# Optimization experiments

Hardware: AMD Instinct MI355X
Metric: run time of the kernel (lower is better)

The kernel has to match this reference:

```python
import jax, jax.numpy as jnp
import numpy as np

POS_IN, HID, DIR_IN, SIG_OUT, COL_OUT = 63, 128, 27, 1, 3
TOTAL = POS_IN * HID + HID + HID * SIG_OUT + SIG_OUT + (HID + DIR_IN) * COL_OUT + COL_OUT  # 8717
B, N = 32, 65536


def positional_encoding(x, num_freqs):
    # x: [..., D] -> [..., D + D*2*num_freqs]
    freqs = 2.0 ** jnp.arange(num_freqs, dtype=x.dtype)  # [F]
    x_exp = x[..., None] * freqs                          # [..., D, F]
    flat = x_exp.reshape(*x.shape[:-1], -1)               # [..., D*F]
    return jnp.concatenate([x, jnp.sin(flat), jnp.cos(flat)], axis=-1)


def setup_inputs() -> dict:
    key = jax.random.key(0)
    k1, k2, k3 = jax.random.split(key, 3)
    params = jax.random.normal(k1, (B, TOTAL), dtype=jnp.float32) * 0.1
    points = jax.random.uniform(k2, (B, N, 3), dtype=jnp.float32, minval=-1.0, maxval=1.0)
    dirs = jax.random.uniform(k3, (B, N, 3), dtype=jnp.float32, minval=-1.0, maxval=1.0)
    return {"params": params, "points": points, "dirs": dirs}


def _unpack(params):
    b = params.shape[0]
    i = 0
    pw = params[:, i:i + POS_IN * HID].reshape(b, HID, POS_IN); i += POS_IN * HID
    pb = params[:, i:i + HID]; i += HID
    sw = params[:, i:i + HID * SIG_OUT].reshape(b, SIG_OUT, HID); i += HID * SIG_OUT
    sb = params[:, i:i + SIG_OUT]; i += SIG_OUT
    cin = HID + DIR_IN
    cw = params[:, i:i + cin * COL_OUT].reshape(b, COL_OUT, cin); i += cin * COL_OUT
    cb = params[:, i:i + COL_OUT]
    return pw, pb, sw, sb, cw, cb


def reference(params, points, dirs):
    pw, pb, sw, sb, cw, cb = _unpack(params)
    pos_enc = positional_encoding(points, 10)   # [B,N,63]
    dir_enc = positional_encoding(dirs, 4)      # [B,N,27]
    h = jnp.einsum('bni,bhi->bnh', pos_enc, pw) + pb[:, None, :]  # [B,N,128]
    h = jax.nn.relu(h)
    sigma = jnp.einsum('bnh,boh->bno', h, sw) + sb[:, None, :]    # [B,N,1]
    h_dir = jnp.concatenate([h, dir_enc], axis=-1)                # [B,N,155]
    color = jnp.einsum('bnc,boc->bno', h_dir, cw) + cb[:, None, :]  # [B,N,3]
    color = jax.nn.sigmoid(color)
    return jnp.concatenate([color, sigma], axis=-1)               # [B,N,4]
```

## Files before the change

### kernel.cpp

```cpp
#include <hip/hip_runtime.h>

#define POS_IN 63
#define HID 128
#define TOTAL 8789
#define NB 32
#define NPTS 65536

#define PB_OFF 8064
#define SW_OFF 8192
#define SB_OFF 8320
#define CW_OFF 8321
#define CB_OFF 8786

#define BLOCKS_PER_BATCH 32
#define PTS_PER_BLOCK (NPTS / BLOCKS_PER_BATCH)
#define ITERS (PTS_PER_BLOCK / 256)

typedef __attribute__((ext_vector_type(8))) short s16x8;
typedef __attribute__((ext_vector_type(4))) float f32x4;
typedef __bf16 bf16x2 __attribute__((ext_vector_type(2)));

__device__ __forceinline__ unsigned short f2bf(float v) {
    unsigned u = __builtin_bit_cast(unsigned, v);
    unsigned r = 0x7fffu + ((u >> 16) & 1u);
    return (unsigned short)((u + r) >> 16);
}
__device__ __forceinline__ unsigned pk2(float a, float b) {
    bf16x2 v;
    v[0] = (__bf16)a;
    v[1] = (__bf16)b;
    return __builtin_bit_cast(unsigned, v);
}

__global__ __launch_bounds__(256, 2) void nerf_mlp_kernel(
        const float* __restrict__ params,
        const float* __restrict__ points,
        const float* __restrict__ dirs,
        float* __restrict__ out)
{
    __shared__ __align__(16) unsigned char smem[37888];
    unsigned short* stage = (unsigned short*)smem;

    const int tid = threadIdx.x;
    const int lane = tid & 63;
    const int wid = tid >> 6;
    const int b = blockIdx.y;
    const float* P = params + (size_t)b * TOTAL;

    for (int idx = tid; idx < 8064; idx += 256) {
        int n = idx / 63;
        int k = idx - n * 63;
        stage[n * 72 + k] = f2bf(P[idx]);
        if (k == 0) stage[n * 72 + 63] = f2bf(P[PB_OFF + n]);
    }
    __syncthreads();

    const int c = lane & 15;
    const int kg = lane >> 4;

    s16x8 wB[8][2];
    #pragma unroll
    for (int nt = 0; nt < 8; ++nt) {
        #pragma unroll
        for (int kh = 0; kh < 2; ++kh) {
            int n = nt * 16 + c;
            int k = kh * 32 + kg * 8;
            uint4 raw = *(const uint4*)&stage[n * 72 + k];
            wB[nt][kh] = __builtin_bit_cast(s16x8, raw);
        }
    }
    __syncthreads();

    s16x8 wB2[4];
    #pragma unroll
    for (int m = 0; m < 4; ++m) {
        unsigned d0 = 0, d1 = 0, d2 = 0, d3 = 0;
        if (c < 4) {
            const int base = (c == 3) ? SW_OFF : (CW_OFF + c * 155);
            const int h0 = m * 32 + kg * 8;
            d0 = pk2(P[base + h0 + 0], P[base + h0 + 1]);
            d1 = pk2(P[base + h0 + 2], P[base + h0 + 3]);
            d2 = pk2(P[base + h0 + 4], P[base + h0 + 5]);
            d3 = pk2(P[base + h0 + 6], P[base + h0 + 7]);
        }
        uint4 dd = make_uint4(d0, d1, d2, d3);
        wB2[m] = __builtin_bit_cast(s16x8, dd);
    }

    const int ch = lane & 3;
    const float cbias = P[ch < 3 ? (CB_OFF + ch) : SB_OFF];

    unsigned char* encb = smem + wid * 8192;
    unsigned char* hbuf = smem + 32768 + wid * 1280;

    const size_t bpts = (size_t)b * NPTS;
    const int n0b = blockIdx.x * PTS_PER_BLOCK;

    for (int it = 0; it < ITERS; ++it) {
        const int n0 = n0b + it * 256 + wid * 64;
        const int p = n0 + lane;

        const float* pp = points + (bpts + p) * 3;
        float x = pp[0], y = pp[1], z = pp[2];
        const float* dd = dirs + (bpts + p) * 3;
        float dx = dd[0], dy = dd[1], dz = dd[2];

        float e[64];
        e[0] = x; e[1] = y; e[2] = z; e[63] = 1.0f;
        #pragma unroll
        for (int i = 0; i < 3; ++i) {
            float v = (i == 0) ? x : (i == 1) ? y : z;
            float s = __sinf(v), co = __cosf(v);
            e[3 + i * 10] = s; e[33 + i * 10] = co;
            #pragma unroll
            for (int f = 1; f < 10; ++f) {
                float ns = 2.f * s * co;
                float nc = 1.f - 2.f * s * s;
                s = ns; co = nc;
                e[3 + i * 10 + f] = s;
                e[33 + i * 10 + f] = co;
            }
        }

        float cp0 = 0.f, cp1 = 0.f, cp2 = 0.f;
        #pragma unroll
        for (int i = 0; i < 3; ++i) {
            float v = (i == 0) ? dx : (i == 1) ? dy : dz;
            cp0 = fmaf(v, P[CW_OFF + 128 + i], cp0);
            cp1 = fmaf(v, P[CW_OFF + 155 + 128 + i], cp1);
            cp2 = fmaf(v, P[CW_OFF + 310 + 128 + i], cp2);
            float s = __sinf(v), co = __cosf(v);
            #pragma unroll
            for (int f = 0; f < 4; ++f) {
                if (f > 0) {
                    float ns = 2.f * s * co;
                    float nc = 1.f - 2.f * s * s;
                    s = ns; co = nc;
                }
                int si = 128 + 3 + i * 4 + f;
                int ci = 128 + 15 + i * 4 + f;
                cp0 = fmaf(s, P[CW_OFF + si], cp0);
                cp1 = fmaf(s, P[CW_OFF + 155 + si], cp1);
                cp2 = fmaf(s, P[CW_OFF + 310 + si], cp2);
                cp0 = fmaf(co, P[CW_OFF + ci], cp0);
                cp1 = fmaf(co, P[CW_OFF + 155 + ci], cp1);
                cp2 = fmaf(co, P[CW_OFF + 310 + ci], cp2);
            }
        }

        #pragma unroll
        for (int kq = 0; kq < 8; ++kq) {
            uint4 q;
            q.x = pk2(e[kq * 8 + 0], e[kq * 8 + 1]);
            q.y = pk2(e[kq * 8 + 2], e[kq * 8 + 3]);
            q.z = pk2(e[kq * 8 + 4], e[kq * 8 + 5]);
            q.w = pk2(e[kq * 8 + 6], e[kq * 8 + 7]);
            *(uint4*)(encb + kq * 1024 + lane * 16) = q;
        }

        float* outp = out + (bpts + n0) * 4;

        #pragma unroll
        for (int t = 0; t < 4; ++t) {
            uint4 a0r = *(const uint4*)(encb + kg * 1024 + (t * 16 + c) * 16);
            uint4 a1r = *(const uint4*)(encb + (4 + kg) * 1024 + (t * 16 + c) * 16);
            s16x8 A0 = __builtin_bit_cast(s16x8, a0r);
            s16x8 A1 = __builtin_bit_cast(s16x8, a1r);

            f32x4 acc[8];
            #pragma unroll
            for (int nt = 0; nt < 8; ++nt) {
                acc[nt] = (f32x4){0.f, 0.f, 0.f, 0.f};
                acc[nt] = __builtin_amdgcn_mfma_f32_16x16x32_bf16(wB[nt][0], A0, acc[nt], 0, 0, 0);
                acc[nt] = __builtin_amdgcn_mfma_f32_16x16x32_bf16(wB[nt][1], A1, acc[nt], 0, 0, 0);
            }
            #pragma unroll
            for (int nt = 0; nt < 8; ++nt)
                #pragma unroll
                for (int j = 0; j < 4; ++j)
                    acc[nt][j] = fmaxf(acc[nt][j], 0.f);

            f32x4 acc2 = (f32x4){0.f, 0.f, 0.f, 0.f};
            #pragma unroll
            for (int m = 0; m < 4; ++m) {
                unsigned q0 = pk2(acc[2 * m][0], acc[2 * m][1]);
                unsigned q1 = pk2(acc[2 * m][2], acc[2 * m][3]);
                unsigned q2 = pk2(acc[2 * m + 1][0], acc[2 * m + 1][1]);
                unsigned q3 = pk2(acc[2 * m + 1][2], acc[2 * m + 1][3]);
                *(uint2*)(hbuf + c * 80 + kg * 8)      = make_uint2(q0, q1);
                *(uint2*)(hbuf + c * 80 + 32 + kg * 8) = make_uint2(q2, q3);
                uint4 ar = *(const uint4*)(hbuf + c * 80 + kg * 16);
                s16x8 A2 = __builtin_bit_cast(s16x8, ar);
                acc2 = __builtin_amdgcn_mfma_f32_16x16x32_bf16(A2, wB2[m], acc2, 0, 0, 0);
            }

            if (c < 4) {
                #pragma unroll
                for (int j = 0; j < 4; ++j)
                    ((float*)hbuf)[(kg * 4 + j) * 4 + c] = acc2[j];
            }
            float v = ((float*)hbuf)[lane];

            int src = t * 16 + (lane >> 2);
            float p0 = __shfl(cp0, src, 64);
            float p1 = __shfl(cp1, src, 64);
            float p2 = __shfl(cp2, src, 64);
            float cpv = (ch == 0) ? p0 : (ch == 1) ? p1 : (ch == 2) ? p2 : 0.f;

            v += cpv + cbias;
            float sig = 1.f / (1.f + __expf(-v));
            v = (ch < 3) ? sig : v;

            outp[t * 64 + lane] = v;
        }
    }
}

extern "C" void kernel_launch(void* const* d_in, const int* in_sizes, int n_in,
                              void* d_out, int out_size, void* d_ws, size_t ws_size,
                              hipStream_t stream) {
    const float* params = (const float*)d_in[0];
    const float* points = (const float*)d_in[1];
    const float* dirs   = (const float*)d_in[2];
    float* out = (float*)d_out;
    dim3 grid(BLOCKS_PER_BATCH, NB);
    nerf_mlp_kernel<<<grid, 256, 0, stream>>>(params, points, dirs, out);
}
```

Before: 90.77 us.

## Cut register pressure: split layer-1 MFMA into halves, move layer-2 weights to LDS

Layer-1 MFMA accumulation is split into two halves of four tiles each, with ReLU and the layer-2 MFMA applied per half, so only 16 accumulator registers are live instead of 32. The layer-2 weights (sigma and color rows) are staged once into shared memory and reloaded per MFMA instead of being held in registers. The hbuf stride shrinks from 80 to 64 bytes to make room, and the launch-bounds occupancy hint is dropped. This trades extra LDS reads and possible bank conflicts from the tighter stride for fewer VGPRs and potentially higher occupancy.

```diff
diff --git a/kernel.cpp b/kernel.cpp
--- a/kernel.cpp
+++ b/kernel.cpp
@@ -32,7 +32,7 @@
     return __builtin_bit_cast(unsigned, v);
 }
 
-__global__ __launch_bounds__(256, 2) void nerf_mlp_kernel(
+__global__ __launch_bounds__(256) void nerf_mlp_kernel(
         const float* __restrict__ params,
         const float* __restrict__ points,
         const float* __restrict__ dirs,
@@ -69,29 +69,28 @@
             wB[nt][kh] = __builtin_bit_cast(s16x8, raw);
         }
     }
+
+    unsigned char* wb2 = smem + 36864;
+    if (wid == 0 && c < 4) {
+        const int base = (c == 3) ? SW_OFF : (CW_OFF + c * 155);
+        #pragma unroll
+        for (int m = 0; m < 4; ++m) {
+            const int h0 = m * 32 + kg * 8;
+            uint4 dd;
+            dd.x = pk2(P[base + h0 + 0], P[base + h0 + 1]);
+            dd.y = pk2(P[base + h0 + 2], P[base + h0 + 3]);
+            dd.z = pk2(P[base + h0 + 4], P[base + h0 + 5]);
+            dd.w = pk2(P[base + h0 + 6], P[base + h0 + 7]);
+            *(uint4*)(wb2 + m * 256 + c * 64 + kg * 16) = dd;
+        }
+    }
     __syncthreads();
-
-    s16x8 wB2[4];
-    #pragma unroll
-    for (int m = 0; m < 4; ++m) {
-        unsigned d0 = 0, d1 = 0, d2 = 0, d3 = 0;
-        if (c < 4) {
-            const int base = (c == 3) ? SW_OFF : (CW_OFF + c * 155);
-            const int h0 = m * 32 + kg * 8;
-            d0 = pk2(P[base + h0 + 0], P[base + h0 + 1]);
-            d1 = pk2(P[base + h0 + 2], P[base + h0 + 3]);
-            d2 = pk2(P[base + h0 + 4], P[base + h0 + 5]);
-            d3 = pk2(P[base + h0 + 6], P[base + h0 + 7]);
-        }
-        uint4 dd = make_uint4(d0, d1, d2, d3);
-        wB2[m] = __builtin_bit_cast(s16x8, dd);
-    }
 
     const int ch = lane & 3;
     const float cbias = P[ch < 3 ? (CB_OFF + ch) : SB_OFF];
 
     unsigned char* encb = smem + wid * 8192;
-    unsigned char* hbuf = smem + 32768 + wid * 1280;
+    unsigned char* hbuf = smem + 32768 + wid * 1024;
 
     const size_t bpts = (size_t)b * NPTS;
     const int n0b = blockIdx.x * PTS_PER_BLOCK;
@@ -167,31 +166,39 @@
             s16x8 A0 = __builtin_bit_cast(s16x8, a0r);
             s16x8 A1 = __builtin_bit_cast(s16x8, a1r);
 
-            f32x4 acc[8];
+            f32x4 acc2 = (f32x4){0.f, 0.f, 0.f, 0.f};
+
             #pragma unroll
-            for (int nt = 0; nt < 8; ++nt) {
-                acc[nt] = (f32x4){0.f, 0.f, 0.f, 0.f};
-                acc[nt] = __builtin_amdgcn_mfma_f32_16x16x32_bf16(wB[nt][0], A0, acc[nt], 0, 0, 0);
-                acc[nt] = __builtin_amdgcn_mfma_f32_16x16x32_bf16(wB[nt][1], A1, acc[nt], 0, 0, 0);
-            }
-            #pragma unroll
-            for (int nt = 0; nt < 8; ++nt)
+            for (int half = 0; half < 2; ++half) {
+                f32x4 acc[4];
                 #pragma unroll
-                for (int j = 0; j < 4; ++j)
-                    acc[nt][j] = fmaxf(acc[nt][j], 0.f);
-
-            f32x4 acc2 = (f32x4){0.f, 0.f, 0.f, 0.f};
-            #pragma unroll
-            for (int m = 0; m < 4; ++m) {
-                unsigned q0 = pk2(acc[2 * m][0], acc[2 * m][1]);
-                unsigned q1 = pk2(acc[2 * m][2], acc[2 * m][3]);
-                unsigned q2 = pk2(acc[2 * m + 1][0], acc[2 * m + 1][1]);
-                unsigned q3 = pk2(acc[2 * m + 1][2], acc[2 * m + 1][3]);
-                *(uint2*)(hbuf + c * 80 + kg * 8)      = make_uint2(q0, q1);
-                *(uint2*)(hbuf + c * 80 + 32 + kg * 8) = make_uint2(q2, q3);
-                uint4 ar = *(const uint4*)(hbuf + c * 80 + kg * 16);
-                s16x8 A2 = __builtin_bit_cast(s16x8, ar);
-                acc2 = __builtin_amdgcn_mfma_f32_16x16x32_bf16(A2, wB2[m], acc2, 0, 0, 0);
+                for (int nt = 0; nt < 4; ++nt) {
+                    acc[nt] = (f32x4){0.f, 0.f, 0.f, 0.f};
+                    acc[nt] = __builtin_amdgcn_mfma_f32_16x16x32_bf16(wB[half * 4 + nt][0], A0, acc[nt], 0, 0, 0);
+                    acc[nt] = __builtin_amdgcn_mfma_f32_16x16x32_bf16(wB[half * 4 + nt][1], A1, acc[nt], 0, 0, 0);
+                    #pragma unroll
+                    for (int j = 0; j < 4; ++j)
+                        acc[nt][j] = fmaxf(acc[nt][j], 0.f);
+                }
+
+                #pragma unroll
+                for (int lm = 0; lm < 2; ++lm) {
+                    const int m = half * 2 + lm;
+                    unsigned q0 = pk2(acc[2 * lm][0], acc[2 * lm][1]);
+                    unsigned q1 = pk2(acc[2 * lm][2], acc[2 * lm][3]);
+                    unsigned q2 = pk2(acc[2 * lm + 1][0], acc[2 * lm + 1][1]);
+                    unsigned q3 = pk2(acc[2 * lm + 1][2], acc[2 * lm + 1][3]);
+                    *(uint2*)(hbuf + c * 64 + kg * 8)      = make_uint2(q0, q1);
+                    *(uint2*)(hbuf + c * 64 + 32 + kg * 8) = make_uint2(q2, q3);
+                    uint4 ar = *(const uint4*)(hbuf + c * 64 + kg * 16);
+                    s16x8 A2 = __builtin_bit_cast(s16x8, ar);
+                    s16x8 B2 = (s16x8){0, 0, 0, 0, 0, 0, 0, 0};
+                    if (c < 4) {
+                        uint4 br = *(const uint4*)(wb2 + m * 256 + c * 64 + kg * 16);
+                        B2 = __builtin_bit_cast(s16x8, br);
+                    }
+                    acc2 = __builtin_amdgcn_mfma_f32_16x16x32_bf16(A2, B2, acc2, 0, 0, 0);
+                }
             }
 
             if (c < 4) {
```

Result: slower. 129.6 us (+42.8%).
